# Optimization experiments

Hardware: AMD Instinct MI355X
Metric: run time of the kernel (lower is better)

Reference implementation:

```python
import jax, jax.numpy as jnp
import numpy as np

B, S, D, E, K = 4, 2048, 1024, 8, 2
H = 4 * D


def setup_inputs() -> dict:
    key = jax.random.key(0)
    k0, k1, k2, k3 = jax.random.split(key, 4)
    x = jax.random.normal(k0, (B, S, D), dtype=jnp.float32)
    router_w = jax.random.normal(k1, (E, D), dtype=jnp.float32) * 0.02
    w1 = jax.random.normal(k2, (E, H, D), dtype=jnp.float32) * 0.02  # fc1 weight [out,in]
    w2 = jax.random.normal(k3, (E, D, H), dtype=jnp.float32) * 0.02  # fc2 weight [out,in]
    return {"x": x, "router_w": router_w, "w1": w1, "w2": w2}


def reference(x, router_w, w1, w2):
    b, s, d = x.shape
    e = router_w.shape[0]
    # Router: logits = x @ router_w.T (nn.Linear, bias=False)
    logits = jnp.einsum('bsd,ed->bse', x, router_w)
    probs = jax.nn.softmax(logits, axis=-1)
    topk_vals, topk_idx = jax.lax.top_k(probs, K)  # [b,s,K]

    x_flat = x.reshape(b * s, d)                  # [T, D]
    vals = topk_vals.reshape(b * s, K)            # [T, K]
    idx = topk_idx.reshape(b * s, K)              # [T, K]

    out = jnp.zeros_like(x_flat)
    # Small fixed loop over experts (8); each token gets summed routing weight
    # for this expert over its K slots (equivalent to the torch per-slot scatter-add).
    for eid in range(e):
        w = jnp.sum(jnp.where(idx == eid, vals, jnp.zeros((), x.dtype)), axis=-1)  # [T]
        h = jax.nn.gelu(x_flat @ w1[eid].T, approximate=False)  # [T, H], exact GELU like F.gelu
        y = h @ w2[eid].T                                        # [T, D]
        out = out + w[:, None] * y
    return out.reshape(b, s, d)
```

## Files before the change

kernel.cpp:

```cpp
#include <hip/hip_runtime.h>
#include <hip/hip_bf16.h>
#include <cstdint>

#define TN 8192
#define DN 1024
#define HN 4096
#define EN 8
#define PADMAX 18432

typedef __attribute__((ext_vector_type(8))) short short8;
typedef __attribute__((ext_vector_type(4))) float f32x4;
typedef __attribute__((ext_vector_type(4))) unsigned short ushort4v;

__device__ inline unsigned short f2bf(float f) {
  unsigned u = __builtin_bit_cast(unsigned, f);
  u = u + 0x7fffu + ((u >> 16) & 1u);
  return (unsigned short)(u >> 16);
}
__device__ inline float bf2f(unsigned short u) {
  unsigned v = ((unsigned)u) << 16;
  return __builtin_bit_cast(float, v);
}

__device__ inline float gelu_f(float v) {
  float z2 = 1.5957691216057308f * (v + 0.044715f * v * v * v);
  return v / (1.f + __expf(-z2));
}

__device__ inline void gload_lds16(const void* g, void* l) {
  __builtin_amdgcn_global_load_lds(
      (const __attribute__((address_space(1))) unsigned int*)g,
      (__attribute__((address_space(3))) unsigned int*)l, 16, 0, 0);
}

__global__ __launch_bounds__(256) void prep_k(const float* __restrict__ x,
                                              const float* __restrict__ rw,
                                              const float* __restrict__ w1,
                                              const float* __restrict__ w2,
                                              unsigned short* __restrict__ xb,
                                              unsigned short* __restrict__ w1b,
                                              unsigned short* __restrict__ w2b,
                                              int* __restrict__ eids,
                                              float* __restrict__ wts,
                                              int nCvtBlk, long nGroups) {
  if (blockIdx.x < TN / 4) {
    int wid = threadIdx.x >> 6, lane = threadIdx.x & 63;
    int t = blockIdx.x * 4 + wid;
    const float* xr = x + (long)t * DN;
    float a[EN];
#pragma unroll
    for (int e = 0; e < EN; ++e) a[e] = 0.f;
    for (int k = lane; k < DN; k += 64) {
      float xv = xr[k];
#pragma unroll
      for (int e = 0; e < EN; ++e) a[e] += xv * rw[e * DN + k];
    }
#pragma unroll
    for (int off = 32; off > 0; off >>= 1) {
#pragma unroll
      for (int e = 0; e < EN; ++e) a[e] += __shfl_xor(a[e], off);
    }
    if (lane == 0) {
      float mx = a[0];
#pragma unroll
      for (int e = 1; e < EN; ++e) mx = fmaxf(mx, a[e]);
      float p[EN], s = 0.f;
#pragma unroll
      for (int e = 0; e < EN; ++e) { p[e] = __expf(a[e] - mx); s += p[e]; }
      int e0 = 0; float b0 = p[0];
#pragma unroll
      for (int e = 1; e < EN; ++e) if (p[e] > b0) { b0 = p[e]; e0 = e; }
      int e1 = -1; float b1 = -1.f;
#pragma unroll
      for (int e = 0; e < EN; ++e) if (e != e0 && p[e] > b1) { b1 = p[e]; e1 = e; }
      float inv = 1.f / s;
      eids[2 * t] = e0; eids[2 * t + 1] = e1;
      wts[2 * t] = b0 * inv; wts[2 * t + 1] = b1 * inv;
    }
  } else {
    const long GX = (long)TN * DN / 8;
    const long GW = (long)EN * HN * DN / 8;
    long g = (long)(blockIdx.x - TN / 4) * 256 + threadIdx.x;
    long stride = (long)nCvtBlk * 256;
    for (; g < nGroups; g += stride) {
      const float* s; unsigned short* d; long j;
      if (g < GX) { s = x; d = xb; j = g; }
      else if (g < GX + GW) { s = w1; d = w1b; j = g - GX; }
      else { s = w2; d = w2b; j = g - GX - GW; }
      long e8 = j * 8;
      float4 v0 = *(const float4*)(s + e8);
      float4 v1 = *(const float4*)(s + e8 + 4);
      short8 pk;
      pk[0] = (short)f2bf(v0.x); pk[1] = (short)f2bf(v0.y);
      pk[2] = (short)f2bf(v0.z); pk[3] = (short)f2bf(v0.w);
      pk[4] = (short)f2bf(v1.x); pk[5] = (short)f2bf(v1.y);
      pk[6] = (short)f2bf(v1.z); pk[7] = (short)f2bf(v1.w);
      *(short8*)(d + e8) = pk;
    }
  }
}

__global__ __launch_bounds__(1024) void count_k(const int* __restrict__ eids,
                                                int* __restrict__ poff) {
  __shared__ int hist[16][EN];
  int tid = threadIdx.x, lane = tid & 63, w = tid >> 6;
  int c[EN];
#pragma unroll
  for (int e = 0; e < EN; ++e) c[e] = 0;
  for (int i = tid; i < 2 * TN; i += 1024) {
    int e = eids[i];
#pragma unroll
    for (int j = 0; j < EN; ++j) c[j] += (e == j) ? 1 : 0;
  }
#pragma unroll
  for (int j = 0; j < EN; ++j) {
#pragma unroll
    for (int off = 32; off > 0; off >>= 1) c[j] += __shfl_xor(c[j], off);
  }
  if (lane == 0) {
#pragma unroll
    for (int j = 0; j < EN; ++j) hist[w][j] = c[j];
  }
  __syncthreads();
  if (tid == 0) {
    int o = 0;
    for (int e = 0; e < EN; ++e) {
      int s = 0;
      for (int ww = 0; ww < 16; ++ww) s += hist[ww][e];
      poff[e] = o;
      o += (s + 127) & ~127;
    }
    poff[EN] = o;
  }
}

__global__ __launch_bounds__(256) void scatter_k(const int* __restrict__ eids,
                                                 const float* __restrict__ wts,
                                                 const int* __restrict__ poff,
                                                 int* __restrict__ cursor,
                                                 int* __restrict__ pairTok,
                                                 float* __restrict__ pairW,
                                                 int* __restrict__ slotPos) {
  int t = blockIdx.x * 256 + threadIdx.x;
#pragma unroll
  for (int k = 0; k < 2; ++k) {
    int e = eids[2 * t + k];
    int p = atomicAdd(&cursor[e], 1);
    int pos = poff[e] + p;
    pairTok[pos] = t;
    pairW[pos] = wts[2 * t + k];
    slotPos[2 * t + k] = pos;
  }
}

__global__ __launch_bounds__(256) void combine_k(const unsigned short* __restrict__ yb,
                                                 const float* __restrict__ wts,
                                                 const int* __restrict__ slotPos,
                                                 float* __restrict__ out) {
  int t = blockIdx.x;
  int p0 = slotPos[2 * t], p1 = slotPos[2 * t + 1];
  float w0 = wts[2 * t], w1 = wts[2 * t + 1];
  int c = threadIdx.x * 4;
  ushort4v y0 = *(const ushort4v*)(yb + (long)p0 * DN + c);
  ushort4v y1 = *(const ushort4v*)(yb + (long)p1 * DN + c);
  float4 o;
  o.x = w0 * bf2f(y0.x) + w1 * bf2f(y1.x);
  o.y = w0 * bf2f(y0.y) + w1 * bf2f(y1.y);
  o.z = w0 * bf2f(y0.z) + w1 * bf2f(y1.z);
  o.w = w0 * bf2f(y0.w) + w1 * bf2f(y1.w);
  *(float4*)(out + (long)t * DN + c) = o;
}


#define BAR() { asm volatile("" ::: "memory"); __builtin_amdgcn_s_barrier(); \
                asm volatile("" ::: "memory"); }
#define LGKM0() { asm volatile("s_waitcnt lgkmcnt(0)" ::: "memory"); }

#define LDA4(PAR) { const char* _b = smem + (PAR)*16384;                             \
  _Pragma("unroll") for (int m = 0; m < 4; ++m) {                                    \
    int row = waveM*64 + m*16 + (lane & 15); int cb = row * 128;                     \
    a[m][0] = *(const short8*)(_b + cb + (((lane>>4) ^ (row&7)) * 16));              \
    a[m][1] = *(const short8*)(_b + cb + (((4 + (lane>>4)) ^ (row&7)) * 16)); } }

#define LDB2(NH, PAR) { const char* _b = smem + 32768 + (PAR)*16384;                 \
  _Pragma("unroll") for (int n = 0; n < 2; ++n) {                                    \
    int row = waveN*64 + ((NH)*2+n)*16 + (lane & 15); int cb = row * 128;            \
    b[(NH)*2+n][0] = *(const short8*)(_b + cb + (((lane>>4) ^ (row&7)) * 16));       \
    b[(NH)*2+n][1] = *(const short8*)(_b + cb + (((4 + (lane>>4)) ^ (row&7)) * 16)); } }

#define MM16(NH) { __builtin_amdgcn_s_setprio(1);                                    \
  _Pragma("unroll") for (int m = 0; m < 4; ++m)                                      \
    _Pragma("unroll") for (int n = 0; n < 2; ++n) {                                  \
      acc[m][(NH)*2+n] = __builtin_amdgcn_mfma_f32_16x16x32_bf16(                    \
          a[m][0], b[(NH)*2+n][0], acc[m][(NH)*2+n], 0, 0, 0);                       \
      acc[m][(NH)*2+n] = __builtin_amdgcn_mfma_f32_16x16x32_bf16(                    \
          a[m][1], b[(NH)*2+n][1], acc[m][(NH)*2+n], 0, 0, 0); }                     \
  __builtin_amdgcn_s_setprio(0); }

template <int MODE, bool BBF16>
__global__ __launch_bounds__(256, 2) void moe_gemm128_k(
    const unsigned short* __restrict__ Ab, const void* __restrict__ Bsrc,
    void* __restrict__ OutP, const int* __restrict__ pairTok,
    const float* __restrict__ pairW, const int* __restrict__ poff, int chunkStart) {
  constexpr int KD = (MODE == 1) ? DN : HN;
  constexpr int ND = (MODE == 1) ? HN : DN;
  constexpr int SPLIT = (MODE == 3) ? 2 : 1;
  constexpr int KLEN = KD / SPLIT;
  constexpr int NT = KLEN / 64;

  extern __shared__ char smem[];

  int NX = gridDim.x;
  int NXY = NX * gridDim.y;
  int orig = blockIdx.y * NX + blockIdx.x;
  int qq = NXY >> 3, rrm = NXY & 7;
  int xcd = orig & 7, pos = orig >> 3;
  int wg = (xcd < rrm ? xcd * (qq + 1) : rrm * (qq + 1) + (xcd - rrm) * qq) + pos;

  int NYt = NXY / NX;
  const int GH = 8;
  int npg = GH * NX;
  int gid = wg / npg;
  int rem = wg - gid * npg;
  int rowsLeft = NYt - gid * GH;
  int gh = rowsLeft < GH ? rowsLeft : GH;
  int row = gid * GH + rem % gh;
  int col = rem / gh;
  int tileN = col * 128;
  int tileStart = chunkStart + row * 128;

  int Ppad = poff[EN];
  if (tileStart >= Ppad) return;
  int e = 0;
  while (e < EN - 1 && tileStart >= poff[e + 1]) ++e;

  int tid = threadIdx.x;
  int wid = tid >> 6, lane = tid & 63;
  int waveM = wid >> 1, waveN = wid & 1;
  int kbase = (MODE == 3) ? blockIdx.z * KLEN : 0;

  int r0 = tid >> 3;
  const char* aSrc[4];
  const char* bSrc[4];
#pragma unroll
  for (int j = 0; j < 4; ++j) {
    int rw_ = j * 32 + r0;
    int s = (tid & 7) ^ (rw_ & 7);
    long abase;
    if (MODE == 1) {
      int tok = pairTok[tileStart + rw_];
      if (tok < 0) tok = 0;
      abase = (long)tok * KD;
    } else {
      abase = (long)(tileStart - chunkStart + rw_) * KD;
    }
    aSrc[j] = (const char*)(Ab + abase + kbase + s * 8);
    long bb = (long)e * ND * KD + (long)(tileN + rw_) * KD + kbase + s * 8;
    bSrc[j] = (const char*)Bsrc + bb * (BBF16 ? 2 : 4);
  }

  auto stageA = [&](int k0, int par) {
#pragma unroll
    for (int j = 0; j < 4; ++j)
      gload_lds16(aSrc[j] + (long)k0 * 2, smem + par * 16384 + (j * 256 + tid) * 16);
  };
  auto stageB = [&](int k0, int par) {
    if constexpr (BBF16) {
#pragma unroll
      for (int j = 0; j < 4; ++j)
        gload_lds16(bSrc[j] + (long)k0 * 2, smem + 32768 + par * 16384 + (j * 256 + tid) * 16);
    } else {
#pragma unroll
      for (int j = 0; j < 4; ++j) {
        const float4* pf = (const float4*)(bSrc[j] + (long)k0 * 4);
        float4 v0 = pf[0], v1 = pf[1];
        short8 pk;
        pk[0] = (short)f2bf(v0.x); pk[1] = (short)f2bf(v0.y);
        pk[2] = (short)f2bf(v0.z); pk[3] = (short)f2bf(v0.w);
        pk[4] = (short)f2bf(v1.x); pk[5] = (short)f2bf(v1.y);
        pk[6] = (short)f2bf(v1.z); pk[7] = (short)f2bf(v1.w);
        *(short8*)(smem + 32768 + par * 16384 + (j * 256 + tid) * 16) = pk;
      }
    }
  };

  f32x4 acc[4][4];
#pragma unroll
  for (int m = 0; m < 4; ++m)
#pragma unroll
    for (int n = 0; n < 4; ++n) acc[m][n] = (f32x4){0.f, 0.f, 0.f, 0.f};
  short8 a[4][2], b[4][2];

  stageA(0, 0); stageB(0, 0);
  stageA(64, 1); stageB(64, 1);
  if constexpr (BBF16) {
    asm volatile("s_waitcnt vmcnt(8)" ::: "memory");
  } else {
    asm volatile("s_waitcnt vmcnt(0) lgkmcnt(0)" ::: "memory");
  }
  BAR();

  for (int t = 0; t < NT; ++t) {
    int P = t & 1;
    int k2 = (t + 2) * 64;
    LDA4(P); LDB2(0, P);
    BAR(); LGKM0();
    MM16(0);
    BAR();
    LDB2(1, P);
    if (t + 2 < NT) stageA(k2, P);
    BAR(); LGKM0();
    MM16(1);
    if (t + 2 < NT) stageB(k2, P);
    if (BBF16 && t + 2 < NT) {
      asm volatile("s_waitcnt vmcnt(8)" ::: "memory");
    } else {
      asm volatile("s_waitcnt vmcnt(0)" ::: "memory");
    }
    BAR();
  }

  if (MODE == 1) {
    unsigned short* hbp = (unsigned short*)OutP;
    int rl0 = tileStart - chunkStart + waveM * 64;
#pragma unroll
    for (int m = 0; m < 4; ++m) {
#pragma unroll
      for (int r = 0; r < 4; ++r) {
        int rl = rl0 + m * 16 + (lane >> 4) * 4 + r;
#pragma unroll
        for (int n = 0; n < 4; ++n) {
          int coln = tileN + waveN * 64 + n * 16 + (lane & 15);
          hbp[(long)rl * HN + coln] = f2bf(gelu_f(acc[m][n][r]));
        }
      }
    }
  } else if (MODE == 2) {
    unsigned short* ybp = (unsigned short*)OutP;
#pragma unroll
    for (int m = 0; m < 4; ++m) {
#pragma unroll
      for (int r = 0; r < 4; ++r) {
        int p = tileStart + waveM * 64 + m * 16 + (lane >> 4) * 4 + r;
#pragma unroll
        for (int n = 0; n < 4; ++n) {
          int coln = tileN + waveN * 64 + n * 16 + (lane & 15);
          ybp[(long)p * ND + coln] = f2bf(acc[m][n][r]);
        }
      }
    }
  } else {
    float* outF = (float*)OutP;
#pragma unroll
    for (int m = 0; m < 4; ++m) {
#pragma unroll
      for (int r = 0; r < 4; ++r) {
        int p = tileStart + waveM * 64 + m * 16 + (lane >> 4) * 4 + r;
        int tok = pairTok[p];
        if (tok < 0) continue;
        float wv = pairW[p];
#pragma unroll
        for (int n = 0; n < 4; ++n) {
          int coln = tileN + waveN * 64 + n * 16 + (lane & 15);
          atomicAdd(&outF[(long)tok * DN + coln], wv * acc[m][n][r]);
        }
      }
    }
  }
}

extern "C" void kernel_launch(void* const* d_in, const int* in_sizes, int n_in,
                              void* d_out, int out_size, void* d_ws, size_t ws_size,
                              hipStream_t stream) {
  const float* x = (const float*)d_in[0];
  const float* rw = (const float*)d_in[1];
  const float* w1 = (const float*)d_in[2];
  const float* w2 = (const float*)d_in[3];
  char* W = (char*)d_ws;
  size_t off = 0;
  auto alloc = [&](size_t sz) {
    off = (off + 255) & ~(size_t)255;
    size_t r = off; off += sz; return r;
  };
  size_t ctrlO = alloc(256);
  size_t eidsO = alloc((size_t)TN * 2 * 4);
  size_t wtsO  = alloc((size_t)TN * 2 * 4);
  size_t ptokO = alloc((size_t)PADMAX * 4);
  size_t pwO   = alloc((size_t)PADMAX * 4);
  size_t sposO = alloc((size_t)TN * 2 * 4);
  size_t xbO   = alloc((size_t)TN * DN * 2);
  size_t wB = (size_t)EN * HN * DN * 2;
  size_t afterFixed = (off + 255) & ~(size_t)255;
  bool bw = ws_size >= afterFixed + 2 * wB + (size_t)128 * HN * 2 + 4096;
  size_t w1bO = 0, w2bO = 0;
  if (bw) { w1bO = alloc(wB); w2bO = alloc(wB); }
  size_t ybB = (size_t)PADMAX * DN * 2;
  size_t afterW = (off + 255) & ~(size_t)255;
  bool dense = ws_size >= afterW + ybB + (size_t)128 * HN * 2 + 4096;
  size_t ybO = 0;
  if (dense) ybO = alloc(ybB);
  size_t hbase = (off + 255) & ~(size_t)255;
  size_t avail = ws_size > hbase ? ws_size - hbase : (size_t)128 * HN * 2;
  long Cl = (long)(avail / ((size_t)HN * 2));
  if (Cl > PADMAX) Cl = PADMAX;
  Cl &= ~127l;
  if (Cl < 128) Cl = 128;
  int C = (int)Cl;
  size_t hbO = alloc((size_t)C * HN * 2);
  int nCh = (PADMAX + C - 1) / C;

  int* cursor = (int*)(W + ctrlO);
  int* poff = cursor + 8;
  int* eids = (int*)(W + eidsO);
  float* wts = (float*)(W + wtsO);
  int* pairTok = (int*)(W + ptokO);
  float* pairW = (float*)(W + pwO);
  int* slotPos = (int*)(W + sposO);
  unsigned short* xb = (unsigned short*)(W + xbO);
  unsigned short* hb = (unsigned short*)(W + hbO);
  unsigned short* yb = (unsigned short*)(W + ybO);

  hipFuncSetAttribute(reinterpret_cast<const void*>(moe_gemm128_k<1, true>),
                      hipFuncAttributeMaxDynamicSharedMemorySize, 65536);
  hipFuncSetAttribute(reinterpret_cast<const void*>(moe_gemm128_k<2, true>),
                      hipFuncAttributeMaxDynamicSharedMemorySize, 65536);
  hipFuncSetAttribute(reinterpret_cast<const void*>(moe_gemm128_k<3, true>),
                      hipFuncAttributeMaxDynamicSharedMemorySize, 65536);
  hipFuncSetAttribute(reinterpret_cast<const void*>(moe_gemm128_k<1, false>),
                      hipFuncAttributeMaxDynamicSharedMemorySize, 65536);
  hipFuncSetAttribute(reinterpret_cast<const void*>(moe_gemm128_k<2, false>),
                      hipFuncAttributeMaxDynamicSharedMemorySize, 65536);
  hipFuncSetAttribute(reinterpret_cast<const void*>(moe_gemm128_k<3, false>),
                      hipFuncAttributeMaxDynamicSharedMemorySize, 65536);

  hipMemsetAsync(W + ctrlO, 0, 256, stream);
  hipMemsetAsync(W + ptokO, 0xFF, (size_t)PADMAX * 4, stream);
  if (!dense) hipMemsetAsync(d_out, 0, (size_t)TN * DN * 4, stream);

  const int nCvtBlk = 4096;
  const long GX = (long)TN * DN / 8;
  const long GW = (long)EN * HN * DN / 8;
  long nGroups = GX + (bw ? 2 * GW : 0);
  prep_k<<<TN / 4 + nCvtBlk, 256, 0, stream>>>(
      x, rw, w1, w2, xb,
      bw ? (unsigned short*)(W + w1bO) : nullptr,
      bw ? (unsigned short*)(W + w2bO) : nullptr,
      eids, wts, nCvtBlk, nGroups);
  count_k<<<1, 1024, 0, stream>>>(eids, poff);
  scatter_k<<<TN / 256, 256, 0, stream>>>(eids, wts, poff, cursor, pairTok, pairW, slotPos);

  int Ctiles = C / 128;
  for (int c = 0; c < nCh; ++c) {
    int cs = c * C;
    if (bw) {
      moe_gemm128_k<1, true><<<dim3(HN / 128, Ctiles, 1), 256, 65536, stream>>>(
          xb, W + w1bO, hb, pairTok, pairW, poff, cs);
      if (dense) {
        moe_gemm128_k<2, true><<<dim3(DN / 128, Ctiles, 1), 256, 65536, stream>>>(
            hb, W + w2bO, yb, pairTok, pairW, poff, cs);
      } else {
        moe_gemm128_k<3, true><<<dim3(DN / 128, Ctiles, 2), 256, 65536, stream>>>(
            hb, W + w2bO, d_out, pairTok, pairW, poff, cs);
      }
    } else {
      moe_gemm128_k<1, false><<<dim3(HN / 128, Ctiles, 1), 256, 65536, stream>>>(
          xb, w1, hb, pairTok, pairW, poff, cs);
      if (dense) {
        moe_gemm128_k<2, false><<<dim3(DN / 128, Ctiles, 1), 256, 65536, stream>>>(
            hb, w2, yb, pairTok, pairW, poff, cs);
      } else {
        moe_gemm128_k<3, false><<<dim3(DN / 128, Ctiles, 2), 256, 65536, stream>>>(
            hb, w2, d_out, pairTok, pairW, poff, cs);
      }
    }
  }
  if (dense) {
    combine_k<<<TN, 256, 0, stream>>>(yb, wts, slotPos, (float*)d_out);
  }
}
```

Before: 554.4 us.

## Overlap w2 bf16 conversion with first fc1 GEMM via extra grid slice

Moves the fp32-to-bf16 conversion of w2 out of the prep kernel and into a second z-slice of the first-chunk fc1 GEMM launch. The conversion blocks then run alongside the GEMM tiles instead of serially before them, hiding the memory-bound conversion behind compute. The cost is competition for CUs and memory bandwidth with the GEMM blocks. Correctness relies on the fc2 GEMM being launched after the first fc1 launch completes, which stream ordering guarantees.

Measured after the change: 542.4 us. 2.2% less time.

```diff
diff --git a/kernel.cpp b/kernel.cpp
--- a/kernel.cpp
+++ b/kernel.cpp
@@ -36,10 +36,8 @@
 __global__ __launch_bounds__(256) void prep_k(const float* __restrict__ x,
                                               const float* __restrict__ rw,
                                               const float* __restrict__ w1,
-                                              const float* __restrict__ w2,
                                               unsigned short* __restrict__ xb,
                                               unsigned short* __restrict__ w1b,
-                                              unsigned short* __restrict__ w2b,
                                               int* __restrict__ eids,
                                               float* __restrict__ wts,
                                               int nCvtBlk, long nGroups) {
@@ -79,14 +77,12 @@
     }
   } else {
     const long GX = (long)TN * DN / 8;
-    const long GW = (long)EN * HN * DN / 8;
     long g = (long)(blockIdx.x - TN / 4) * 256 + threadIdx.x;
     long stride = (long)nCvtBlk * 256;
     for (; g < nGroups; g += stride) {
       const float* s; unsigned short* d; long j;
       if (g < GX) { s = x; d = xb; j = g; }
-      else if (g < GX + GW) { s = w1; d = w1b; j = g - GX; }
-      else { s = w2; d = w2b; j = g - GX - GW; }
+      else { s = w1; d = w1b; j = g - GX; }
       long e8 = j * 8;
       float4 v0 = *(const float4*)(s + e8);
       float4 v1 = *(const float4*)(s + e8 + 4);
@@ -201,7 +197,8 @@
 __global__ __launch_bounds__(256, 2) void moe_gemm128_k(
     const unsigned short* __restrict__ Ab, const void* __restrict__ Bsrc,
     void* __restrict__ OutP, const int* __restrict__ pairTok,
-    const float* __restrict__ pairW, const int* __restrict__ poff, int chunkStart) {
+    const float* __restrict__ pairW, const int* __restrict__ poff, int chunkStart,
+    const float* __restrict__ w2src, unsigned short* __restrict__ w2dst) {
   constexpr int KD = (MODE == 1) ? DN : HN;
   constexpr int ND = (MODE == 1) ? HN : DN;
   constexpr int SPLIT = (MODE == 3) ? 2 : 1;
@@ -209,6 +206,25 @@
   constexpr int NT = KLEN / 64;
 
   extern __shared__ char smem[];
+
+  if (MODE == 1 && blockIdx.z == 1) {
+    const long nG = (long)EN * HN * DN / 8;
+    long b = (long)blockIdx.y * gridDim.x + blockIdx.x;
+    long g = b * 256 + threadIdx.x;
+    long stride = (long)gridDim.x * gridDim.y * 256;
+    for (; g < nG; g += stride) {
+      long e8 = g * 8;
+      float4 v0 = *(const float4*)(w2src + e8);
+      float4 v1 = *(const float4*)(w2src + e8 + 4);
+      short8 pk;
+      pk[0] = (short)f2bf(v0.x); pk[1] = (short)f2bf(v0.y);
+      pk[2] = (short)f2bf(v0.z); pk[3] = (short)f2bf(v0.w);
+      pk[4] = (short)f2bf(v1.x); pk[5] = (short)f2bf(v1.y);
+      pk[6] = (short)f2bf(v1.z); pk[7] = (short)f2bf(v1.w);
+      *(short8*)(w2dst + e8) = pk;
+    }
+    return;
+  }
 
   int NX = gridDim.x;
   int NXY = NX * gridDim.y;
@@ -440,11 +456,10 @@
   const int nCvtBlk = 4096;
   const long GX = (long)TN * DN / 8;
   const long GW = (long)EN * HN * DN / 8;
-  long nGroups = GX + (bw ? 2 * GW : 0);
+  long nGroups = GX + (bw ? GW : 0);
   prep_k<<<TN / 4 + nCvtBlk, 256, 0, stream>>>(
-      x, rw, w1, w2, xb,
+      x, rw, w1, xb,
       bw ? (unsigned short*)(W + w1bO) : nullptr,
-      bw ? (unsigned short*)(W + w2bO) : nullptr,
       eids, wts, nCvtBlk, nGroups);
   count_k<<<1, 1024, 0, stream>>>(eids, poff);
   scatter_k<<<TN / 256, 256, 0, stream>>>(eids, wts, poff, cursor, pairTok, pairW, slotPos);
@@ -453,24 +468,25 @@
   for (int c = 0; c < nCh; ++c) {
     int cs = c * C;
     if (bw) {
-      moe_gemm128_k<1, true><<<dim3(HN / 128, Ctiles, 1), 256, 65536, stream>>>(
-          xb, W + w1bO, hb, pairTok, pairW, poff, cs);
+      moe_gemm128_k<1, true><<<dim3(HN / 128, Ctiles, c == 0 ? 2 : 1), 256, 65536, stream>>>(
+          xb, W + w1bO, hb, pairTok, pairW, poff, cs, w2,
+          (unsigned short*)(W + w2bO));
       if (dense) {
         moe_gemm128_k<2, true><<<dim3(DN / 128, Ctiles, 1), 256, 65536, stream>>>(
-            hb, W + w2bO, yb, pairTok, pairW, poff, cs);
+            hb, W + w2bO, yb, pairTok, pairW, poff, cs, nullptr, nullptr);
       } else {
         moe_gemm128_k<3, true><<<dim3(DN / 128, Ctiles, 2), 256, 65536, stream>>>(
-            hb, W + w2bO, d_out, pairTok, pairW, poff, cs);
+            hb, W + w2bO, d_out, pairTok, pairW, poff, cs, nullptr, nullptr);
       }
     } else {
       moe_gemm128_k<1, false><<<dim3(HN / 128, Ctiles, 1), 256, 65536, stream>>>(
-          xb, w1, hb, pairTok, pairW, poff, cs);
+          xb, w1, hb, pairTok, pairW, poff, cs, nullptr, nullptr);
       if (dense) {
         moe_gemm128_k<2, false><<<dim3(DN / 128, Ctiles, 1), 256, 65536, stream>>>(
-            hb, w2, yb, pairTok, pairW, poff, cs);
+            hb, w2, yb, pairTok, pairW, poff, cs, nullptr, nullptr);
       } else {
         moe_gemm128_k<3, false><<<dim3(DN / 128, Ctiles, 2), 256, 65536, stream>>>(
-            hb, w2, d_out, pairTok, pairW, poff, cs);
+            hb, w2, d_out, pairTok, pairW, poff, cs, nullptr, nullptr);
       }
     }
   }
```
